# Kernel optimization log

Measured on AMD Instinct MI355X. Metric: run time of the kernel, lower is better.

## Reference

```python
import jax, jax.numpy as jnp
import numpy as np

B, T, R = 128, 20, 49           # batch, caption length, num regions (7x7)
V, E, H, FD, A = 10000, 512, 512, 512, 256  # vocab, embed, hidden, feature, attn dims


def setup_inputs() -> dict:
    key = jax.random.key(0)
    ks = jax.random.split(key, 16)
    s = 0.02
    return {
        "features": jax.random.normal(ks[0], (B, R, FD), dtype=jnp.float32),
        "captions": jax.random.randint(ks[1], (B, T), 0, V),
        "emb": jax.random.normal(ks[2], (V, E), dtype=jnp.float32) * s,
        "W_h": jax.random.normal(ks[3], (A, H), dtype=jnp.float32) * s,
        "b_h": jnp.zeros((A,), jnp.float32),
        "W_f": jax.random.normal(ks[4], (A, FD), dtype=jnp.float32) * s,
        "b_f": jnp.zeros((A,), jnp.float32),
        "v_w": jax.random.normal(ks[5], (A,), dtype=jnp.float32) * s,
        "v_b": jnp.zeros((), jnp.float32),
        "W_ih": jax.random.normal(ks[6], (4 * H, E + FD), dtype=jnp.float32) * s,
        "W_hh": jax.random.normal(ks[7], (4 * H, H), dtype=jnp.float32) * s,
        "b_ih": jnp.zeros((4 * H,), jnp.float32),
        "b_hh": jnp.zeros((4 * H,), jnp.float32),
        "fc_W": jax.random.normal(ks[8], (V, H), dtype=jnp.float32) * s,
        "fc_b": jnp.zeros((V,), jnp.float32),
    }


def reference(features, captions, emb, W_h, b_h, W_f, b_f, v_w, v_b,
              W_ih, W_hh, b_ih, b_hh, fc_W, fc_b):
    Bn = features.shape[0]
    Hd = W_hh.shape[1]
    # features are constant across timesteps -> project once (same math as per-step W_f(features))
    f_proj = jnp.einsum('brf,af->bra', features, W_f) + b_f  # (B,R,A)
    embeds = emb[captions[:, :-1]]                            # (B,T-1,E)
    xs = jnp.swapaxes(embeds, 0, 1)                           # (T-1,B,E)
    bias = b_ih + b_hh

    def step(carry, x_t):
        hx, cx = carry
        # Bahdanau attention
        h = hx @ W_h.T + b_h                                  # (B,A)
        scores = jnp.tanh(h[:, None, :] + f_proj) @ v_w + v_b  # (B,R)
        alpha = jax.nn.softmax(scores, axis=1)
        context = jnp.einsum('br,brf->bf', alpha, features)   # (B,FD)
        # LSTMCell (PyTorch gate order: i,f,g,o)
        lstm_in = jnp.concatenate([x_t, context], axis=1)     # (B,E+FD)
        gates = lstm_in @ W_ih.T + hx @ W_hh.T + bias         # (B,4H)
        i, f, g, o = jnp.split(gates, 4, axis=1)
        cx = jax.nn.sigmoid(f) * cx + jax.nn.sigmoid(i) * jnp.tanh(g)
        hx = jax.nn.sigmoid(o) * jnp.tanh(cx)
        logit = hx @ fc_W.T + fc_b                            # (B,V)
        return (hx, cx), logit

    init = (jnp.zeros((Bn, Hd), features.dtype), jnp.zeros((Bn, Hd), features.dtype))
    _, logits = jax.lax.scan(step, init, xs)                  # (T-1,B,V)
    return jnp.swapaxes(logits, 0, 1)                         # (B,T-1,V)
```

## Files before the change

### kernel.cpp

```cpp
#include <hip/hip_runtime.h>
#include <hip/hip_bf16.h>
#include <math.h>

#define NB 128
#define NT 20
#define NS 19
#define NR 49
#define NV 10000
#define NE 512
#define NH 512
#define NFD 512
#define NA 256
#define NG 2048
#define NKC 1536

typedef __bf16 bf16_t;
typedef bf16_t bf16x8 __attribute__((ext_vector_type(8)));
typedef float f32x4 __attribute__((ext_vector_type(4)));

__device__ __forceinline__ float sigm(float x) { return 1.f / (1.f + expf(-x)); }

__global__ __launch_bounds__(256) void k_setup(
    const float* __restrict__ W_ih, const float* __restrict__ W_hh,
    const float* __restrict__ b_ih, const float* __restrict__ b_hh,
    const float* __restrict__ W_h, const float* __restrict__ fc_W,
    const float* __restrict__ W_f, const float* __restrict__ features,
    bf16_t* __restrict__ Wcatb, bf16_t* __restrict__ fcWb,
    bf16_t* __restrict__ Wfb, bf16_t* __restrict__ featb,
    bf16_t* __restrict__ W_hb, float* __restrict__ bias,
    float* __restrict__ hx, float* __restrict__ cx)
{
    int idx = blockIdx.x * 256 + threadIdx.x;
    if (idx < NV * NH) fcWb[idx] = (bf16_t)fc_W[idx];
    if (idx < NG * NKC) {
        int n = idx / NKC, k = idx % NKC;
        int h = n >> 2, g = n & 3;
        int orig = g * NH + h;
        Wcatb[idx] = (bf16_t)((k < NE + NFD) ? W_ih[orig * (NE + NFD) + k]
                                             : W_hh[orig * NH + (k - NE - NFD)]);
    }
    if (idx < NB * NR * NFD) featb[idx] = (bf16_t)features[idx];
    if (idx < NA * NFD) Wfb[idx] = (bf16_t)W_f[idx];
    if (idx < NA * NH) W_hb[idx] = (bf16_t)W_h[idx];
    if (idx < NG) {
        int h = idx >> 2, g = idx & 3;
        int orig = g * NH + h;
        bias[idx] = b_ih[orig] + b_hh[orig];
    }
    if (idx < NB * NH) { hx[idx] = 0.f; cx[idx] = 0.f; }
}

__global__ __launch_bounds__(1024) void k_attn(
    const float* __restrict__ hx, const bf16_t* __restrict__ W_hb,
    const float* __restrict__ b_h, const float* __restrict__ fproj,
    const float* __restrict__ v_w, const bf16_t* __restrict__ featb,
    const float* __restrict__ emb, const int* __restrict__ captions,
    bf16_t* __restrict__ lin, int t)
{
    int b = blockIdx.x;
    int tid = threadIdx.x;
    __shared__ float hxs[NH];
    __shared__ float part[4][NA];
    __shared__ float hatt[NA];
    __shared__ float salpha[64];

    if (tid < NH) hxs[tid] = hx[b * NH + tid];
    __syncthreads();

    {
        int a = tid & (NA - 1), q = tid >> 8;
        const bf16x8* wrow = (const bf16x8*)(W_hb + (size_t)a * NH + q * 128);
        const float* hq = hxs + q * 128;
        float p = 0.f;
        #pragma unroll
        for (int c = 0; c < 16; ++c) {
            bf16x8 wv = wrow[c];
            int k = c * 8;
            p += hq[k+0]*(float)wv[0] + hq[k+1]*(float)wv[1]
               + hq[k+2]*(float)wv[2] + hq[k+3]*(float)wv[3]
               + hq[k+4]*(float)wv[4] + hq[k+5]*(float)wv[5]
               + hq[k+6]*(float)wv[6] + hq[k+7]*(float)wv[7];
        }
        part[q][a] = p;
    }
    __syncthreads();
    if (tid < NA)
        hatt[tid] = part[0][tid] + part[1][tid] + part[2][tid] + part[3][tid] + b_h[tid];
    __syncthreads();

    {
        int wv = tid >> 6, lane = tid & 63;
        for (int r = wv; r < NR; r += 16) {
            float s = 0.f;
            const float* fp = fproj + (size_t)(b * NR + r) * NA;
            #pragma unroll
            for (int j = 0; j < 4; ++j) {
                int aa = lane + 64 * j;
                s += tanhf(hatt[aa] + fp[aa]) * v_w[aa];
            }
            #pragma unroll
            for (int off = 32; off; off >>= 1) s += __shfl_xor(s, off);
            if (lane == 0) salpha[r] = s;
        }
    }
    __syncthreads();

    if (tid < 64) {
        float v = (tid < NR) ? salpha[tid] : -INFINITY;
        float m = v;
        #pragma unroll
        for (int off = 32; off; off >>= 1) m = fmaxf(m, __shfl_xor(m, off));
        float e = (tid < NR) ? expf(v - m) : 0.f;
        float ssum = e;
        #pragma unroll
        for (int off = 32; off; off >>= 1) ssum += __shfl_xor(ssum, off);
        if (tid < NR) salpha[tid] = e / ssum;
    }
    __syncthreads();

    if (tid < NH) {
        bf16_t* lrow = lin + (size_t)b * NKC;
        lrow[tid] = (bf16_t)emb[(size_t)captions[b * NT + t] * NE + tid];
        lrow[NE + NFD + tid] = (bf16_t)hxs[tid];
        float c = 0.f;
        #pragma unroll 7
        for (int r = 0; r < NR; ++r)
            c += salpha[r] * (float)featb[(size_t)(b * NR + r) * NFD + tid];
        lrow[NE + tid] = (bf16_t)c;
    }
}

__global__ __launch_bounds__(256) void gemm_bf16_nt(
    const bf16_t* __restrict__ Am, const bf16_t* __restrict__ Bm,
    const float* __restrict__ bias, float* __restrict__ Cm,
    int M, int N, int K, int ldc)
{
    __shared__ uint4 AsU[512];
    __shared__ uint4 BsU[512];
    int tid = threadIdx.x;
    int m0 = blockIdx.x * 64, n0 = blockIdx.y * 64;
    int nk = K >> 6;

    int rowS = tid >> 3, slotS = tid & 7;
    int wr0 = rowS * 8 + (slotS ^ (rowS & 7));
    int rowS2 = rowS + 32;
    int wr1 = rowS2 * 8 + (slotS ^ (rowS2 & 7));

    const uint4* pA = (const uint4*)(Am + (size_t)(m0 + rowS) * K) + slotS;
    size_t aStep = (size_t)4 * K;
    int nrow0 = n0 + rowS, nrow1 = n0 + rowS2;
    bool bv0 = nrow0 < N, bv1 = nrow1 < N;
    const uint4* pB0 = (const uint4*)(Bm + (size_t)nrow0 * K) + slotS;
    const uint4* pB1 = (const uint4*)(Bm + (size_t)nrow1 * K) + slotS;
    uint4 zz = make_uint4(0, 0, 0, 0);

    int w = tid >> 6, lane = tid & 63;
    int wm = w >> 1, wn = w & 1;
    int lr = lane & 15, lg = lane >> 4;
    int ra[2][2], rb[2][2];
    #pragma unroll
    for (int i = 0; i < 2; ++i)
        #pragma unroll
        for (int kk = 0; kk < 2; ++kk) {
            int rA = wm * 32 + i * 16 + lr;
            int rB = wn * 32 + i * 16 + lr;
            int s = kk * 4 + lg;
            ra[i][kk] = rA * 8 + (s ^ (rA & 7));
            rb[i][kk] = rB * 8 + (s ^ (rB & 7));
        }

    f32x4 acc00 = {}, acc01 = {}, acc10 = {}, acc11 = {};
    uint4 a0 = pA[0], a1 = pA[aStep];
    uint4 b0 = bv0 ? pB0[0] : zz;
    uint4 b1 = bv1 ? pB1[0] : zz;
    pA += 8; pB0 += 8; pB1 += 8;

    for (int kt = 0; kt < nk; ++kt) {
        __syncthreads();
        AsU[wr0] = a0; AsU[wr1] = a1;
        BsU[wr0] = b0; BsU[wr1] = b1;
        if (kt + 1 < nk) {
            a0 = pA[0]; a1 = pA[aStep];
            b0 = bv0 ? pB0[0] : zz;
            b1 = bv1 ? pB1[0] : zz;
            pA += 8; pB0 += 8; pB1 += 8;
        }
        __syncthreads();
        const bf16x8* Af = (const bf16x8*)AsU;
        const bf16x8* Bf = (const bf16x8*)BsU;
        #pragma unroll
        for (int kk = 0; kk < 2; ++kk) {
            bf16x8 fa0 = Af[ra[0][kk]], fa1 = Af[ra[1][kk]];
            bf16x8 fb0 = Bf[rb[0][kk]], fb1 = Bf[rb[1][kk]];
            acc00 = __builtin_amdgcn_mfma_f32_16x16x32_bf16(fa0, fb0, acc00, 0, 0, 0);
            acc01 = __builtin_amdgcn_mfma_f32_16x16x32_bf16(fa0, fb1, acc01, 0, 0, 0);
            acc10 = __builtin_amdgcn_mfma_f32_16x16x32_bf16(fa1, fb0, acc10, 0, 0, 0);
            acc11 = __builtin_amdgcn_mfma_f32_16x16x32_bf16(fa1, fb1, acc11, 0, 0, 0);
        }
    }

    f32x4 av[2][2] = {{acc00, acc01}, {acc10, acc11}};
    #pragma unroll
    for (int i = 0; i < 2; ++i) {
        int mbase = m0 + wm * 32 + i * 16 + lg * 4;
        #pragma unroll
        for (int j = 0; j < 2; ++j) {
            int n = n0 + wn * 32 + j * 16 + lr;
            if (n < N) {
                float bz = bias ? bias[n] : 0.f;
                #pragma unroll
                for (int r = 0; r < 4; ++r)
                    Cm[(size_t)(mbase + r) * ldc + n] = av[i][j][r] + bz;
            }
        }
    }
}

__global__ __launch_bounds__(256) void k_step(
    const bf16_t* __restrict__ lin, const bf16_t* __restrict__ Wcatb,
    const float* __restrict__ bias, float* __restrict__ hx,
    float* __restrict__ cx, bf16_t* __restrict__ hxAll, int t)
{
    __shared__ __align__(16) char smem[16640];
    uint4* AsU = (uint4*)smem;
    uint4* BsU = AsU + 512;

    int tid = threadIdx.x;
    int m0 = blockIdx.x * 64, n0 = blockIdx.y * 64;

    int rowS = tid >> 3, slotS = tid & 7;
    int wr0 = rowS * 8 + (slotS ^ (rowS & 7));
    int rowS2 = rowS + 32;
    int wr1 = rowS2 * 8 + (slotS ^ (rowS2 & 7));

    const uint4* pA = (const uint4*)(lin + (size_t)(m0 + rowS) * NKC) + slotS;
    const uint4* pB0 = (const uint4*)(Wcatb + (size_t)(n0 + rowS) * NKC) + slotS;
    const uint4* pB1 = (const uint4*)(Wcatb + (size_t)(n0 + rowS2) * NKC) + slotS;
    size_t aStep = (size_t)4 * NKC;

    int w = tid >> 6, lane = tid & 63;
    int wm = w >> 1, wn = w & 1;
    int lr = lane & 15, lg = lane >> 4;
    int ra[2][2], rb[2][2];
    #pragma unroll
    for (int i = 0; i < 2; ++i)
        #pragma unroll
        for (int kk = 0; kk < 2; ++kk) {
            int rA = wm * 32 + i * 16 + lr;
            int rB = wn * 32 + i * 16 + lr;
            int s = kk * 4 + lg;
            ra[i][kk] = rA * 8 + (s ^ (rA & 7));
            rb[i][kk] = rB * 8 + (s ^ (rB & 7));
        }

    f32x4 acc00 = {}, acc01 = {}, acc10 = {}, acc11 = {};
    uint4 a0 = pA[0], a1 = pA[aStep];
    uint4 b0 = pB0[0], b1 = pB1[0];
    pA += 8; pB0 += 8; pB1 += 8;

    #pragma unroll 1
    for (int kt = 0; kt < NKC / 64; ++kt) {
        __syncthreads();
        AsU[wr0] = a0; AsU[wr1] = a1;
        BsU[wr0] = b0; BsU[wr1] = b1;
        if (kt + 1 < NKC / 64) {
            a0 = pA[0]; a1 = pA[aStep];
            b0 = pB0[0]; b1 = pB1[0];
            pA += 8; pB0 += 8; pB1 += 8;
        }
        __syncthreads();
        const bf16x8* Af = (const bf16x8*)AsU;
        const bf16x8* Bf = (const bf16x8*)BsU;
        #pragma unroll
        for (int kk = 0; kk < 2; ++kk) {
            bf16x8 fa0 = Af[ra[0][kk]], fa1 = Af[ra[1][kk]];
            bf16x8 fb0 = Bf[rb[0][kk]], fb1 = Bf[rb[1][kk]];
            acc00 = __builtin_amdgcn_mfma_f32_16x16x32_bf16(fa0, fb0, acc00, 0, 0, 0);
            acc01 = __builtin_amdgcn_mfma_f32_16x16x32_bf16(fa0, fb1, acc01, 0, 0, 0);
            acc10 = __builtin_amdgcn_mfma_f32_16x16x32_bf16(fa1, fb0, acc10, 0, 0, 0);
            acc11 = __builtin_amdgcn_mfma_f32_16x16x32_bf16(fa1, fb1, acc11, 0, 0, 0);
        }
    }

    __syncthreads();
    float* Ct = (float*)smem;
    f32x4 av[2][2] = {{acc00, acc01}, {acc10, acc11}};
    #pragma unroll
    for (int i = 0; i < 2; ++i)
        #pragma unroll
        for (int j = 0; j < 2; ++j) {
            int mloc = wm * 32 + i * 16 + lg * 4;
            int nloc = wn * 32 + j * 16 + lr;
            #pragma unroll
            for (int r = 0; r < 4; ++r)
                Ct[(mloc + r) * 65 + nloc] = av[i][j][r];
        }
    __syncthreads();

    int hloc = tid & 15;
    int h = (n0 >> 2) + hloc;
    #pragma unroll
    for (int q = 0; q < 4; ++q) {
        int m = (tid >> 4) + q * 16;
        int b = m0 + m;
        const float* crow = Ct + m * 65 + hloc * 4;
        const float* brow = bias + n0 + hloc * 4;
        float gi = crow[0] + brow[0];
        float gf = crow[1] + brow[1];
        float gg = crow[2] + brow[2];
        float go = crow[3] + brow[3];
        size_t idx = (size_t)b * NH + h;
        float c = sigm(gf) * cx[idx] + sigm(gi) * tanhf(gg);
        float hn = sigm(go) * tanhf(c);
        cx[idx] = c;
        hx[idx] = hn;
        hxAll[((size_t)t * NB + b) * NH + h] = (bf16_t)hn;
    }
}

__global__ __launch_bounds__(256) void k_logits(
    const bf16_t* __restrict__ hxAll, const bf16_t* __restrict__ fcWb,
    const float* __restrict__ fc_b, float* __restrict__ out)
{
    __shared__ uint4 AsU[512];
    __shared__ uint4 BsU[512];
    int tid = threadIdx.x;
    int m0 = blockIdx.x * 64, n0 = blockIdx.y * 64;

    int rowS = tid >> 3, slotS = tid & 7;
    int wr0 = rowS * 8 + (slotS ^ (rowS & 7));
    int rowS2 = rowS + 32;
    int wr1 = rowS2 * 8 + (slotS ^ (rowS2 & 7));

    const uint4* pA = (const uint4*)(hxAll + (size_t)(m0 + rowS) * NH) + slotS;
    size_t aStep = (size_t)4 * NH;
    int nrow0 = n0 + rowS, nrow1 = n0 + rowS2;
    bool bv0 = nrow0 < NV, bv1 = nrow1 < NV;
    const uint4* pB0 = (const uint4*)(fcWb + (size_t)nrow0 * NH) + slotS;
    const uint4* pB1 = (const uint4*)(fcWb + (size_t)nrow1 * NH) + slotS;
    uint4 zz = make_uint4(0, 0, 0, 0);

    int w = tid >> 6, lane = tid & 63;
    int wm = w >> 1, wn = w & 1;
    int lr = lane & 15, lg = lane >> 4;
    int ra[2][2], rb[2][2];
    #pragma unroll
    for (int i = 0; i < 2; ++i)
        #pragma unroll
        for (int kk = 0; kk < 2; ++kk) {
            int rA = wm * 32 + i * 16 + lr;
            int rB = wn * 32 + i * 16 + lr;
            int s = kk * 4 + lg;
            ra[i][kk] = rA * 8 + (s ^ (rA & 7));
            rb[i][kk] = rB * 8 + (s ^ (rB & 7));
        }

    f32x4 acc00 = {}, acc01 = {}, acc10 = {}, acc11 = {};
    uint4 a0 = pA[0], a1 = pA[aStep];
    uint4 b0 = bv0 ? pB0[0] : zz;
    uint4 b1 = bv1 ? pB1[0] : zz;
    pA += 8; pB0 += 8; pB1 += 8;

    #pragma unroll 1
    for (int kt = 0; kt < NH / 64; ++kt) {
        __syncthreads();
        AsU[wr0] = a0; AsU[wr1] = a1;
        BsU[wr0] = b0; BsU[wr1] = b1;
        if (kt + 1 < NH / 64) {
            a0 = pA[0]; a1 = pA[aStep];
            b0 = bv0 ? pB0[0] : zz;
            b1 = bv1 ? pB1[0] : zz;
            pA += 8; pB0 += 8; pB1 += 8;
        }
        __syncthreads();
        const bf16x8* Af = (const bf16x8*)AsU;
        const bf16x8* Bf = (const bf16x8*)BsU;
        #pragma unroll
        for (int kk = 0; kk < 2; ++kk) {
            bf16x8 fa0 = Af[ra[0][kk]], fa1 = Af[ra[1][kk]];
            bf16x8 fb0 = Bf[rb[0][kk]], fb1 = Bf[rb[1][kk]];
            acc00 = __builtin_amdgcn_mfma_f32_16x16x32_bf16(fa0, fb0, acc00, 0, 0, 0);
            acc01 = __builtin_amdgcn_mfma_f32_16x16x32_bf16(fa0, fb1, acc01, 0, 0, 0);
            acc10 = __builtin_amdgcn_mfma_f32_16x16x32_bf16(fa1, fb0, acc10, 0, 0, 0);
            acc11 = __builtin_amdgcn_mfma_f32_16x16x32_bf16(fa1, fb1, acc11, 0, 0, 0);
        }
    }

    f32x4 av[2][2] = {{acc00, acc01}, {acc10, acc11}};
    #pragma unroll
    for (int i = 0; i < 2; ++i) {
        int mbase = m0 + wm * 32 + i * 16 + lg * 4;
        #pragma unroll
        for (int j = 0; j < 2; ++j) {
            int n = n0 + wn * 32 + j * 16 + lr;
            if (n < NV) {
                float bz = fc_b[n];
                #pragma unroll
                for (int r = 0; r < 4; ++r) {
                    int m = mbase + r;
                    int b = m & 127, tt = m >> 7;
                    out[((size_t)b * NS + tt) * NV + n] = av[i][j][r] + bz;
                }
            }
        }
    }
}

extern "C" void kernel_launch(void* const* d_in, const int* in_sizes, int n_in,
                              void* d_out, int out_size, void* d_ws, size_t ws_size,
                              hipStream_t stream)
{
    const float* features = (const float*)d_in[0];
    const int*   captions = (const int*)d_in[1];
    const float* emb      = (const float*)d_in[2];
    const float* W_h      = (const float*)d_in[3];
    const float* b_h      = (const float*)d_in[4];
    const float* W_f      = (const float*)d_in[5];
    const float* b_f      = (const float*)d_in[6];
    const float* v_w      = (const float*)d_in[7];
    const float* W_ih     = (const float*)d_in[9];
    const float* W_hh     = (const float*)d_in[10];
    const float* b_ih     = (const float*)d_in[11];
    const float* b_hh     = (const float*)d_in[12];
    const float* fc_W     = (const float*)d_in[13];
    const float* fc_b     = (const float*)d_in[14];
    float* out = (float*)d_out;

    char* base = (char*)d_ws;
    bf16_t* Wcatb = (bf16_t*)base;  base += (size_t)NG * NKC * 2;
    bf16_t* fcWb  = (bf16_t*)base;  base += (size_t)NV * NH * 2;
    bf16_t* Wfb   = (bf16_t*)base;  base += (size_t)NA * NFD * 2;
    bf16_t* featb = (bf16_t*)base;  base += (size_t)NB * NR * NFD * 2;
    bf16_t* lin   = (bf16_t*)base;  base += (size_t)NB * NKC * 2;
    bf16_t* W_hb  = (bf16_t*)base;  base += (size_t)NA * NH * 2;
    bf16_t* hxAll = (bf16_t*)base;  base += (size_t)NS * NB * NH * 2;
    float* bias   = (float*)base;   base += (size_t)NG * 4;
    float* fproj  = (float*)base;   base += (size_t)NB * NR * NA * 4;
    float* hx     = (float*)base;   base += (size_t)NB * NH * 4;
    float* cx     = (float*)base;   base += (size_t)NB * NH * 4;

    k_setup<<<dim3((NV * NH + 255) / 256), 256, 0, stream>>>(
        W_ih, W_hh, b_ih, b_hh, W_h, fc_W, W_f, features,
        Wcatb, fcWb, Wfb, featb, W_hb, bias, hx, cx);

    gemm_bf16_nt<<<dim3(98, 4), 256, 0, stream>>>(
        featb, Wfb, b_f, fproj, NB * NR, NA, NFD, NA);

    for (int t = 0; t < NS; ++t) {
        k_attn<<<dim3(NB), 1024, 0, stream>>>(
            hx, W_hb, b_h, fproj, v_w, featb, emb, captions, lin, t);
        k_step<<<dim3(2, 32), 256, 0, stream>>>(
            lin, Wcatb, bias, hx, cx, hxAll, t);
    }

    k_logits<<<dim3(38, 157), 256, 0, stream>>>(hxAll, fcWb, fc_b, out);
}
```

Measured before the change: 682.5 us.

## Hoist embedding gate projection out of the recurrence; retile logits GEMM; vectorise prep

The embedding part of the LSTM input projection (W_ih[:, :512] times the embeddings) no longer runs inside each step. It is now one batched GEMM over all timesteps, stored as bf16 pre-activations, which shrinks the per-step K from 1536 to 1024. The logits GEMM moves to 128x128 tiles with an XCD-aware block swizzle. The setup kernel now converts with 8-wide vector loads, the attention kernel uses 512 threads, and the embedding gather moves into prep. Storing the precomputed gate contribution in bf16 adds some rounding error.

```diff
diff --git a/kernel.cpp b/kernel.cpp
--- a/kernel.cpp
+++ b/kernel.cpp
@@ -12,7 +12,7 @@
 #define NFD 512
 #define NA 256
 #define NG 2048
-#define NKC 1536
+#define NK2 1024
 
 typedef __bf16 bf16_t;
 typedef bf16_t bf16x8 __attribute__((ext_vector_type(8)));
@@ -20,120 +20,84 @@
 
 __device__ __forceinline__ float sigm(float x) { return 1.f / (1.f + expf(-x)); }
 
-__global__ __launch_bounds__(256) void k_setup(
-    const float* __restrict__ W_ih, const float* __restrict__ W_hh,
+__device__ __forceinline__ void cvt8(bf16_t* d, const float* s) {
+    float4 a = *(const float4*)s;
+    float4 b = *(const float4*)(s + 4);
+    bf16x8 v;
+    v[0] = (bf16_t)a.x; v[1] = (bf16_t)a.y; v[2] = (bf16_t)a.z; v[3] = (bf16_t)a.w;
+    v[4] = (bf16_t)b.x; v[5] = (bf16_t)b.y; v[6] = (bf16_t)b.z; v[7] = (bf16_t)b.w;
+    *(bf16x8*)d = v;
+}
+
+__global__ __launch_bounds__(256) void k_prep(
+    const float* __restrict__ fc_W, const float* __restrict__ W_ih,
+    const float* __restrict__ W_hh, const float* __restrict__ W_h,
+    const float* __restrict__ W_f, const float* __restrict__ features,
+    const float* __restrict__ emb, const int* __restrict__ captions,
     const float* __restrict__ b_ih, const float* __restrict__ b_hh,
-    const float* __restrict__ W_h, const float* __restrict__ fc_W,
-    const float* __restrict__ W_f, const float* __restrict__ features,
-    bf16_t* __restrict__ Wcatb, bf16_t* __restrict__ fcWb,
+    bf16_t* __restrict__ fcWb, bf16_t* __restrict__ Wcat2,
+    bf16_t* __restrict__ Wxg, bf16_t* __restrict__ W_hb,
     bf16_t* __restrict__ Wfb, bf16_t* __restrict__ featb,
-    bf16_t* __restrict__ W_hb, float* __restrict__ bias,
+    bf16_t* __restrict__ linx, float* __restrict__ bias,
     float* __restrict__ hx, float* __restrict__ cx)
 {
-    int idx = blockIdx.x * 256 + threadIdx.x;
-    if (idx < NV * NH) fcWb[idx] = (bf16_t)fc_W[idx];
-    if (idx < NG * NKC) {
-        int n = idx / NKC, k = idx % NKC;
-        int h = n >> 2, g = n & 3;
-        int orig = g * NH + h;
-        Wcatb[idx] = (bf16_t)((k < NE + NFD) ? W_ih[orig * (NE + NFD) + k]
-                                             : W_hh[orig * NH + (k - NE - NFD)]);
-    }
-    if (idx < NB * NR * NFD) featb[idx] = (bf16_t)features[idx];
-    if (idx < NA * NFD) Wfb[idx] = (bf16_t)W_f[idx];
-    if (idx < NA * NH) W_hb[idx] = (bf16_t)W_h[idx];
-    if (idx < NG) {
-        int h = idx >> 2, g = idx & 3;
-        int orig = g * NH + h;
-        bias[idx] = b_ih[orig] + b_hh[orig];
-    }
-    if (idx < NB * NH) { hx[idx] = 0.f; cx[idx] = 0.f; }
-}
-
-__global__ __launch_bounds__(1024) void k_attn(
-    const float* __restrict__ hx, const bf16_t* __restrict__ W_hb,
-    const float* __restrict__ b_h, const float* __restrict__ fproj,
-    const float* __restrict__ v_w, const bf16_t* __restrict__ featb,
-    const float* __restrict__ emb, const int* __restrict__ captions,
-    bf16_t* __restrict__ lin, int t)
-{
-    int b = blockIdx.x;
-    int tid = threadIdx.x;
-    __shared__ float hxs[NH];
-    __shared__ float part[4][NA];
-    __shared__ float hatt[NA];
-    __shared__ float salpha[64];
-
-    if (tid < NH) hxs[tid] = hx[b * NH + tid];
-    __syncthreads();
-
-    {
-        int a = tid & (NA - 1), q = tid >> 8;
-        const bf16x8* wrow = (const bf16x8*)(W_hb + (size_t)a * NH + q * 128);
-        const float* hq = hxs + q * 128;
-        float p = 0.f;
-        #pragma unroll
-        for (int c = 0; c < 16; ++c) {
-            bf16x8 wv = wrow[c];
-            int k = c * 8;
-            p += hq[k+0]*(float)wv[0] + hq[k+1]*(float)wv[1]
-               + hq[k+2]*(float)wv[2] + hq[k+3]*(float)wv[3]
-               + hq[k+4]*(float)wv[4] + hq[k+5]*(float)wv[5]
-               + hq[k+6]*(float)wv[6] + hq[k+7]*(float)wv[7];
-        }
-        part[q][a] = p;
-    }
-    __syncthreads();
-    if (tid < NA)
-        hatt[tid] = part[0][tid] + part[1][tid] + part[2][tid] + part[3][tid] + b_h[tid];
-    __syncthreads();
-
-    {
-        int wv = tid >> 6, lane = tid & 63;
-        for (int r = wv; r < NR; r += 16) {
-            float s = 0.f;
-            const float* fp = fproj + (size_t)(b * NR + r) * NA;
-            #pragma unroll
-            for (int j = 0; j < 4; ++j) {
-                int aa = lane + 64 * j;
-                s += tanhf(hatt[aa] + fp[aa]) * v_w[aa];
-            }
-            #pragma unroll
-            for (int off = 32; off; off >>= 1) s += __shfl_xor(s, off);
-            if (lane == 0) salpha[r] = s;
-        }
-    }
-    __syncthreads();
-
-    if (tid < 64) {
-        float v = (tid < NR) ? salpha[tid] : -INFINITY;
-        float m = v;
-        #pragma unroll
-        for (int off = 32; off; off >>= 1) m = fmaxf(m, __shfl_xor(m, off));
-        float e = (tid < NR) ? expf(v - m) : 0.f;
-        float ssum = e;
-        #pragma unroll
-        for (int off = 32; off; off >>= 1) ssum += __shfl_xor(ssum, off);
-        if (tid < NR) salpha[tid] = e / ssum;
-    }
-    __syncthreads();
-
-    if (tid < NH) {
-        bf16_t* lrow = lin + (size_t)b * NKC;
-        lrow[tid] = (bf16_t)emb[(size_t)captions[b * NT + t] * NE + tid];
-        lrow[NE + NFD + tid] = (bf16_t)hxs[tid];
-        float c = 0.f;
-        #pragma unroll 7
-        for (int r = 0; r < NR; ++r)
-            c += salpha[r] * (float)featb[(size_t)(b * NR + r) * NFD + tid];
-        lrow[NE + tid] = (bf16_t)c;
-    }
+    int g = blockIdx.x * 256 + threadIdx.x;
+    if (g < 640000) { int idx = g * 8; cvt8(fcWb + idx, fc_W + idx); return; }
+    g -= 640000;
+    if (g < 262144) {
+        int idx = g * 8;
+        int row = idx >> 10, col = idx & 1023;
+        int orig = (row & 3) * NH + (row >> 2);
+        const float* src = (col < 512) ? (W_ih + (size_t)orig * 1024 + 512 + col)
+                                       : (W_hh + (size_t)orig * 512 + (col - 512));
+        cvt8(Wcat2 + idx, src);
+        return;
+    }
+    g -= 262144;
+    if (g < 131072) {
+        int idx = g * 8;
+        int row = idx >> 9, col = idx & 511;
+        int orig = (row & 3) * NH + (row >> 2);
+        cvt8(Wxg + idx, W_ih + (size_t)orig * 1024 + col);
+        return;
+    }
+    g -= 131072;
+    if (g < 16384) { int idx = g * 8; cvt8(W_hb + idx, W_h + idx); return; }
+    g -= 16384;
+    if (g < 16384) { int idx = g * 8; cvt8(Wfb + idx, W_f + idx); return; }
+    g -= 16384;
+    if (g < 401408) { int idx = g * 8; cvt8(featb + idx, features + idx); return; }
+    g -= 401408;
+    if (g < 155648) {
+        int idx = g * 8;
+        int row = idx >> 9, col = idx & 511;
+        int t = row >> 7, b = row & 127;
+        int cap = captions[b * NT + t];
+        cvt8(linx + idx, emb + (size_t)cap * NE + col);
+        return;
+    }
+    g -= 155648;
+    if (g < 256) {
+        int n0 = g * 8;
+        #pragma unroll
+        for (int i = 0; i < 8; ++i) {
+            int n = n0 + i, h = n >> 2, gg = n & 3;
+            int orig = gg * NH + h;
+            bias[n] = b_ih[orig] + b_hh[orig];
+        }
+        return;
+    }
+    g -= 256;
+    float4 z = make_float4(0.f, 0.f, 0.f, 0.f);
+    if (g < 8192) { *(float4*)(hx + g * 8) = z; *(float4*)(hx + g * 8 + 4) = z; return; }
+    g -= 8192;
+    if (g < 8192) { *(float4*)(cx + g * 8) = z; *(float4*)(cx + g * 8 + 4) = z; }
 }
 
 __global__ __launch_bounds__(256) void gemm_bf16_nt(
     const bf16_t* __restrict__ Am, const bf16_t* __restrict__ Bm,
-    const float* __restrict__ bias, float* __restrict__ Cm,
-    int M, int N, int K, int ldc)
+    const float* __restrict__ bias, float* __restrict__ Cf,
+    bf16_t* __restrict__ Cb, int M, int N, int K, int ldc)
 {
     __shared__ uint4 AsU[512];
     __shared__ uint4 BsU[512];
@@ -175,6 +139,7 @@
     uint4 b1 = bv1 ? pB1[0] : zz;
     pA += 8; pB0 += 8; pB1 += 8;
 
+    #pragma unroll 1
     for (int kt = 0; kt < nk; ++kt) {
         __syncthreads();
         AsU[wr0] = a0; AsU[wr1] = a1;
@@ -209,17 +174,96 @@
             if (n < N) {
                 float bz = bias ? bias[n] : 0.f;
                 #pragma unroll
-                for (int r = 0; r < 4; ++r)
-                    Cm[(size_t)(mbase + r) * ldc + n] = av[i][j][r] + bz;
+                for (int r = 0; r < 4; ++r) {
+                    float v = av[i][j][r] + bz;
+                    if (Cb) Cb[(size_t)(mbase + r) * ldc + n] = (bf16_t)v;
+                    else    Cf[(size_t)(mbase + r) * ldc + n] = v;
+                }
             }
         }
     }
 }
 
+__global__ __launch_bounds__(512) void k_attn(
+    const float* __restrict__ hx, const bf16_t* __restrict__ W_hb,
+    const float* __restrict__ b_h, const float* __restrict__ fproj,
+    const float* __restrict__ v_w, const bf16_t* __restrict__ featb,
+    bf16_t* __restrict__ lin)
+{
+    int b = blockIdx.x;
+    int tid = threadIdx.x;
+    int w = tid >> 6, lane = tid & 63;
+    __shared__ float hxs[NH];
+    __shared__ float part[2][NA];
+    __shared__ float salpha[64];
+
+    hxs[tid] = hx[b * NH + tid];
+    __syncthreads();
+
+    {
+        int a = tid & 255, q = tid >> 8;
+        const bf16x8* wrow = (const bf16x8*)(W_hb + (size_t)a * NH + q * 256);
+        const float* hq = hxs + q * 256;
+        float p = 0.f;
+        #pragma unroll
+        for (int c = 0; c < 32; ++c) {
+            bf16x8 wv = wrow[c];
+            int k = c * 8;
+            p += hq[k+0]*(float)wv[0] + hq[k+1]*(float)wv[1]
+               + hq[k+2]*(float)wv[2] + hq[k+3]*(float)wv[3]
+               + hq[k+4]*(float)wv[4] + hq[k+5]*(float)wv[5]
+               + hq[k+6]*(float)wv[6] + hq[k+7]*(float)wv[7];
+        }
+        part[q][a] = p;
+    }
+    __syncthreads();
+
+    {
+        for (int r = w; r < NR; r += 8) {
+            const float* fp = fproj + ((size_t)b * NR + r) * NA;
+            float s = 0.f;
+            #pragma unroll
+            for (int j = 0; j < 4; ++j) {
+                int aa = lane + 64 * j;
+                float hv = part[0][aa] + part[1][aa] + b_h[aa];
+                s += tanhf(hv + fp[aa]) * v_w[aa];
+            }
+            #pragma unroll
+            for (int off = 32; off; off >>= 1) s += __shfl_xor(s, off);
+            if (lane == 0) salpha[r] = s;
+        }
+    }
+    __syncthreads();
+
+    if (tid < 64) {
+        float v = (tid < NR) ? salpha[tid] : -INFINITY;
+        float m = v;
+        #pragma unroll
+        for (int off = 32; off; off >>= 1) m = fmaxf(m, __shfl_xor(m, off));
+        float e = (tid < NR) ? expf(v - m) : 0.f;
+        float ssum = e;
+        #pragma unroll
+        for (int off = 32; off; off >>= 1) ssum += __shfl_xor(ssum, off);
+        if (tid < NR) salpha[tid] = e / ssum;
+    }
+    __syncthreads();
+
+    {
+        bf16_t* lrow = lin + (size_t)b * NK2;
+        float c = 0.f;
+        #pragma unroll 7
+        for (int r = 0; r < NR; ++r)
+            c += salpha[r] * (float)featb[((size_t)b * NR + r) * NFD + tid];
+        lrow[tid] = (bf16_t)c;
+        lrow[NFD + tid] = (bf16_t)hxs[tid];
+    }
+}
+
 __global__ __launch_bounds__(256) void k_step(
-    const bf16_t* __restrict__ lin, const bf16_t* __restrict__ Wcatb,
-    const float* __restrict__ bias, float* __restrict__ hx,
-    float* __restrict__ cx, bf16_t* __restrict__ hxAll, int t)
+    const bf16_t* __restrict__ lin, const bf16_t* __restrict__ Wcat2,
+    const bf16_t* __restrict__ pre_x, const float* __restrict__ bias,
+    float* __restrict__ hx, float* __restrict__ cx,
+    bf16_t* __restrict__ hxAll, int t)
 {
     __shared__ __align__(16) char smem[16640];
     uint4* AsU = (uint4*)smem;
@@ -233,10 +277,10 @@
     int rowS2 = rowS + 32;
     int wr1 = rowS2 * 8 + (slotS ^ (rowS2 & 7));
 
-    const uint4* pA = (const uint4*)(lin + (size_t)(m0 + rowS) * NKC) + slotS;
-    const uint4* pB0 = (const uint4*)(Wcatb + (size_t)(n0 + rowS) * NKC) + slotS;
-    const uint4* pB1 = (const uint4*)(Wcatb + (size_t)(n0 + rowS2) * NKC) + slotS;
-    size_t aStep = (size_t)4 * NKC;
+    const uint4* pA = (const uint4*)(lin + (size_t)(m0 + rowS) * NK2) + slotS;
+    const uint4* pB0 = (const uint4*)(Wcat2 + (size_t)(n0 + rowS) * NK2) + slotS;
+    const uint4* pB1 = (const uint4*)(Wcat2 + (size_t)(n0 + rowS2) * NK2) + slotS;
+    size_t aStep = (size_t)4 * NK2;
 
     int w = tid >> 6, lane = tid & 63;
     int wm = w >> 1, wn = w & 1;
@@ -259,11 +303,11 @@
     pA += 8; pB0 += 8; pB1 += 8;
 
     #pragma unroll 1
-    for (int kt = 0; kt < NKC / 64; ++kt) {
+    for (int kt = 0; kt < NK2 / 64; ++kt) {
         __syncthreads();
         AsU[wr0] = a0; AsU[wr1] = a1;
         BsU[wr0] = b0; BsU[wr1] = b1;
-        if (kt + 1 < NKC / 64) {
+        if (kt + 1 < NK2 / 64) {
             a0 = pA[0]; a1 = pA[aStep];
             b0 = pB0[0]; b1 = pB1[0];
             pA += 8; pB0 += 8; pB1 += 8;
@@ -302,19 +346,20 @@
     #pragma unroll
     for (int q = 0; q < 4; ++q) {
         int m = (tid >> 4) + q * 16;
-        int b = m0 + m;
+        int bb = m0 + m;
         const float* crow = Ct + m * 65 + hloc * 4;
         const float* brow = bias + n0 + hloc * 4;
-        float gi = crow[0] + brow[0];
-        float gf = crow[1] + brow[1];
-        float gg = crow[2] + brow[2];
-        float go = crow[3] + brow[3];
-        size_t idx = (size_t)b * NH + h;
+        const bf16_t* prow = pre_x + ((size_t)t * NB + bb) * NG + n0 + hloc * 4;
+        float gi = crow[0] + brow[0] + (float)prow[0];
+        float gf = crow[1] + brow[1] + (float)prow[1];
+        float gg = crow[2] + brow[2] + (float)prow[2];
+        float go = crow[3] + brow[3] + (float)prow[3];
+        size_t idx = (size_t)bb * NH + h;
         float c = sigm(gf) * cx[idx] + sigm(gi) * tanhf(gg);
         float hn = sigm(go) * tanhf(c);
         cx[idx] = c;
         hx[idx] = hn;
-        hxAll[((size_t)t * NB + b) * NH + h] = (bf16_t)hn;
+        hxAll[((size_t)t * NB + bb) * NH + h] = (bf16_t)hn;
     }
 }
 
@@ -322,84 +367,99 @@
     const bf16_t* __restrict__ hxAll, const bf16_t* __restrict__ fcWb,
     const float* __restrict__ fc_b, float* __restrict__ out)
 {
-    __shared__ uint4 AsU[512];
-    __shared__ uint4 BsU[512];
+    const int NWG = 19 * 79, Q = NWG / 8, R = NWG % 8;
+    int bid = blockIdx.x;
+    int xcd = bid & 7, loc = bid >> 3;
+    int swz = (xcd < R ? xcd * (Q + 1) : R * (Q + 1) + (xcd - R) * Q) + loc;
+    int m0 = (swz % 19) * 128;
+    int n0 = (swz / 19) * 128;
+
+    __shared__ uint4 AsU[1024];
+    __shared__ uint4 BsU[1024];
     int tid = threadIdx.x;
-    int m0 = blockIdx.x * 64, n0 = blockIdx.y * 64;
 
     int rowS = tid >> 3, slotS = tid & 7;
-    int wr0 = rowS * 8 + (slotS ^ (rowS & 7));
-    int rowS2 = rowS + 32;
-    int wr1 = rowS2 * 8 + (slotS ^ (rowS2 & 7));
+    int wrr[4];
+    #pragma unroll
+    for (int j = 0; j < 4; ++j) {
+        int rj = rowS + 32 * j;
+        wrr[j] = rj * 8 + (slotS ^ (rj & 7));
+    }
 
     const uint4* pA = (const uint4*)(hxAll + (size_t)(m0 + rowS) * NH) + slotS;
-    size_t aStep = (size_t)4 * NH;
-    int nrow0 = n0 + rowS, nrow1 = n0 + rowS2;
-    bool bv0 = nrow0 < NV, bv1 = nrow1 < NV;
-    const uint4* pB0 = (const uint4*)(fcWb + (size_t)nrow0 * NH) + slotS;
-    const uint4* pB1 = (const uint4*)(fcWb + (size_t)nrow1 * NH) + slotS;
+    const uint4* pB = (const uint4*)(fcWb + (size_t)(n0 + rowS) * NH) + slotS;
+    size_t step32 = (size_t)32 * (NH / 8);
+    bool bvv[4];
+    #pragma unroll
+    for (int j = 0; j < 4; ++j) bvv[j] = (n0 + rowS + 32 * j) < NV;
     uint4 zz = make_uint4(0, 0, 0, 0);
 
     int w = tid >> 6, lane = tid & 63;
     int wm = w >> 1, wn = w & 1;
     int lr = lane & 15, lg = lane >> 4;
-    int ra[2][2], rb[2][2];
-    #pragma unroll
-    for (int i = 0; i < 2; ++i)
+    int ra[4][2], rb[4][2];
+    #pragma unroll
+    for (int i = 0; i < 4; ++i)
         #pragma unroll
         for (int kk = 0; kk < 2; ++kk) {
-            int rA = wm * 32 + i * 16 + lr;
-            int rB = wn * 32 + i * 16 + lr;
+            int rA = wm * 64 + i * 16 + lr;
+            int rB = wn * 64 + i * 16 + lr;
             int s = kk * 4 + lg;
             ra[i][kk] = rA * 8 + (s ^ (rA & 7));
             rb[i][kk] = rB * 8 + (s ^ (rB & 7));
         }
 
-    f32x4 acc00 = {}, acc01 = {}, acc10 = {}, acc11 = {};
-    uint4 a0 = pA[0], a1 = pA[aStep];
-    uint4 b0 = bv0 ? pB0[0] : zz;
-    uint4 b1 = bv1 ? pB1[0] : zz;
-    pA += 8; pB0 += 8; pB1 += 8;
+    f32x4 acc[4][4] = {};
+    uint4 aR[4], bR[4];
+    #pragma unroll
+    for (int j = 0; j < 4; ++j) {
+        aR[j] = pA[j * step32];
+        bR[j] = bvv[j] ? pB[j * step32] : zz;
+    }
+    pA += 8; pB += 8;
 
     #pragma unroll 1
     for (int kt = 0; kt < NH / 64; ++kt) {
         __syncthreads();
-        AsU[wr0] = a0; AsU[wr1] = a1;
-        BsU[wr0] = b0; BsU[wr1] = b1;
+        #pragma unroll
+        for (int j = 0; j < 4; ++j) { AsU[wrr[j]] = aR[j]; BsU[wrr[j]] = bR[j]; }
         if (kt + 1 < NH / 64) {
-            a0 = pA[0]; a1 = pA[aStep];
-            b0 = bv0 ? pB0[0] : zz;
-            b1 = bv1 ? pB1[0] : zz;
-            pA += 8; pB0 += 8; pB1 += 8;
+            #pragma unroll
+            for (int j = 0; j < 4; ++j) {
+                aR[j] = pA[j * step32];
+                bR[j] = bvv[j] ? pB[j * step32] : zz;
+            }
+            pA += 8; pB += 8;
         }
         __syncthreads();
         const bf16x8* Af = (const bf16x8*)AsU;
         const bf16x8* Bf = (const bf16x8*)BsU;
         #pragma unroll
         for (int kk = 0; kk < 2; ++kk) {
-            bf16x8 fa0 = Af[ra[0][kk]], fa1 = Af[ra[1][kk]];
-            bf16x8 fb0 = Bf[rb[0][kk]], fb1 = Bf[rb[1][kk]];
-            acc00 = __builtin_amdgcn_mfma_f32_16x16x32_bf16(fa0, fb0, acc00, 0, 0, 0);
-            acc01 = __builtin_amdgcn_mfma_f32_16x16x32_bf16(fa0, fb1, acc01, 0, 0, 0);
-            acc10 = __builtin_amdgcn_mfma_f32_16x16x32_bf16(fa1, fb0, acc10, 0, 0, 0);
-            acc11 = __builtin_amdgcn_mfma_f32_16x16x32_bf16(fa1, fb1, acc11, 0, 0, 0);
-        }
-    }
-
-    f32x4 av[2][2] = {{acc00, acc01}, {acc10, acc11}};
-    #pragma unroll
-    for (int i = 0; i < 2; ++i) {
-        int mbase = m0 + wm * 32 + i * 16 + lg * 4;
-        #pragma unroll
-        for (int j = 0; j < 2; ++j) {
-            int n = n0 + wn * 32 + j * 16 + lr;
+            bf16x8 fa[4], fb[4];
+            #pragma unroll
+            for (int i = 0; i < 4; ++i) { fa[i] = Af[ra[i][kk]]; fb[i] = Bf[rb[i][kk]]; }
+            #pragma unroll
+            for (int i = 0; i < 4; ++i)
+                #pragma unroll
+                for (int j = 0; j < 4; ++j)
+                    acc[i][j] = __builtin_amdgcn_mfma_f32_16x16x32_bf16(fa[i], fb[j], acc[i][j], 0, 0, 0);
+        }
+    }
+
+    #pragma unroll
+    for (int i = 0; i < 4; ++i) {
+        int mbase = m0 + wm * 64 + i * 16 + lg * 4;
+        #pragma unroll
+        for (int j = 0; j < 4; ++j) {
+            int n = n0 + wn * 64 + j * 16 + lr;
             if (n < NV) {
                 float bz = fc_b[n];
                 #pragma unroll
                 for (int r = 0; r < 4; ++r) {
                     int m = mbase + r;
-                    int b = m & 127, tt = m >> 7;
-                    out[((size_t)b * NS + tt) * NV + n] = av[i][j][r] + bz;
+                    int bb = m & 127, tt = m >> 7;
+                    out[((size_t)bb * NS + tt) * NV + n] = acc[i][j][r] + bz;
                 }
             }
         }
@@ -427,31 +487,37 @@
     float* out = (float*)d_out;
 
     char* base = (char*)d_ws;
-    bf16_t* Wcatb = (bf16_t*)base;  base += (size_t)NG * NKC * 2;
     bf16_t* fcWb  = (bf16_t*)base;  base += (size_t)NV * NH * 2;
+    bf16_t* Wcat2 = (bf16_t*)base;  base += (size_t)NG * NK2 * 2;
+    bf16_t* Wxg   = (bf16_t*)base;  base += (size_t)NG * NE * 2;
+    bf16_t* W_hb  = (bf16_t*)base;  base += (size_t)NA * NH * 2;
     bf16_t* Wfb   = (bf16_t*)base;  base += (size_t)NA * NFD * 2;
     bf16_t* featb = (bf16_t*)base;  base += (size_t)NB * NR * NFD * 2;
-    bf16_t* lin   = (bf16_t*)base;  base += (size_t)NB * NKC * 2;
-    bf16_t* W_hb  = (bf16_t*)base;  base += (size_t)NA * NH * 2;
+    bf16_t* linx  = (bf16_t*)base;  base += (size_t)NS * NB * NE * 2;
+    bf16_t* pre_x = (bf16_t*)base;  base += (size_t)NS * NB * NG * 2;
+    bf16_t* lin   = (bf16_t*)base;  base += (size_t)NB * NK2 * 2;
     bf16_t* hxAll = (bf16_t*)base;  base += (size_t)NS * NB * NH * 2;
-    float* bias   = (float*)base;   base += (size_t)NG * 4;
-    float* fproj  = (float*)base;   base += (size_t)NB * NR * NA * 4;
-    float* hx     = (float*)base;   base += (size_t)NB * NH * 4;
-    float* cx     = (float*)base;   base += (size_t)NB * NH * 4;
-
-    k_setup<<<dim3((NV * NH + 255) / 256), 256, 0, stream>>>(
-        W_ih, W_hh, b_ih, b_hh, W_h, fc_W, W_f, features,
-        Wcatb, fcWb, Wfb, featb, W_hb, bias, hx, cx);
+    float*  fproj = (float*)base;   base += (size_t)NB * NR * NA * 4;
+    float*  bias  = (float*)base;   base += (size_t)NG * 4;
+    float*  hx    = (float*)base;   base += (size_t)NB * NH * 4;
+    float*  cx    = (float*)base;   base += (size_t)NB * NH * 4;
+
+    k_prep<<<dim3(6405), 256, 0, stream>>>(
+        fc_W, W_ih, W_hh, W_h, W_f, features, emb, captions, b_ih, b_hh,
+        fcWb, Wcat2, Wxg, W_hb, Wfb, featb, linx, bias, hx, cx);
 
     gemm_bf16_nt<<<dim3(98, 4), 256, 0, stream>>>(
-        featb, Wfb, b_f, fproj, NB * NR, NA, NFD, NA);
+        featb, Wfb, b_f, fproj, (bf16_t*)0, NB * NR, NA, NFD, NA);
+
+    gemm_bf16_nt<<<dim3(38, 32), 256, 0, stream>>>(
+        linx, Wxg, (const float*)0, (float*)0, pre_x, NS * NB, NG, NE, NG);
 
     for (int t = 0; t < NS; ++t) {
-        k_attn<<<dim3(NB), 1024, 0, stream>>>(
-            hx, W_hb, b_h, fproj, v_w, featb, emb, captions, lin, t);
+        k_attn<<<dim3(NB), 512, 0, stream>>>(
+            hx, W_hb, b_h, fproj, v_w, featb, lin);
         k_step<<<dim3(2, 32), 256, 0, stream>>>(
-            lin, Wcatb, bias, hx, cx, hxAll, t);
-    }
-
-    k_logits<<<dim3(38, 157), 256, 0, stream>>>(hxAll, fcWb, fc_b, out);
-}
+            lin, Wcat2, pre_x, bias, hx, cx, hxAll, t);
+    }
+
+    k_logits<<<dim3(19 * 79), 256, 0, stream>>>(hxAll, fcWb, fc_b, out);
+}
```

After: 787.5 us. 15.4% more time.
